# Kernel tuning notes

Measured on AMD Instinct MI355X. Metric: run time of the kernel, lower is better.

The kernel has to match this reference:

```python
import jax, jax.numpy as jnp
import numpy as np

N_NODES = 200000
N_EDGES = 3200000
NUM_GRAPHS = 100
NODES_PER_GRAPH = 2000
D_IN = 128
D_HID = 128
D_OUT = 64


def setup_inputs() -> dict:
    key = jax.random.key(0)
    ks = jax.random.split(key, 8)
    features = jax.random.normal(ks[0], (N_NODES, D_IN), dtype=jnp.float32)
    src = jax.random.randint(ks[1], (N_EDGES,), 0, N_NODES, dtype=jnp.int32)
    dst = jax.random.randint(ks[2], (N_EDGES,), 0, N_NODES, dtype=jnp.int32)
    to_fetch = jax.random.randint(ks[3], (NUM_GRAPHS,), 0, NODES_PER_GRAPH, dtype=jnp.int32)
    w1 = jax.random.normal(ks[4], (D_IN, D_HID), dtype=jnp.float32) * (1.0 / np.sqrt(D_IN))
    b1 = jnp.zeros((D_HID,), dtype=jnp.float32)
    w2 = jax.random.normal(ks[5], (D_HID, D_HID), dtype=jnp.float32) * (1.0 / np.sqrt(D_HID))
    b2 = jnp.zeros((D_HID,), dtype=jnp.float32)
    w3 = jax.random.normal(ks[6], (D_OUT, D_HID), dtype=jnp.float32) * (1.0 / np.sqrt(D_HID))  # F.linear weight [out, in]
    b3 = jnp.zeros((D_OUT,), dtype=jnp.float32)
    return {"features": features, "src": src, "dst": dst, "to_fetch": to_fetch,
            "w1": w1, "b1": b1, "w2": w2, "b2": b2, "w3": w3, "b3": b3}


def _graph_conv(h, src, dst, norm, w, b):
    # DGL GraphConv (in_feats == out_feats branch): normalize, aggregate copy_src/sum, matmul, normalize, bias, relu
    h = h * norm
    agg = jax.ops.segment_sum(h[src], dst, num_segments=N_NODES)  # [N, d]
    rst = jnp.matmul(agg, w) * norm + b
    return jax.nn.relu(rst)


def reference(features, src, dst, to_fetch, w1, b1, w2, b2, w3, b3):
    # in-degree based symmetric-ish norm (DGL uses in_degrees for both sides here)
    deg = jax.ops.segment_sum(jnp.ones((N_EDGES,), jnp.float32), dst, num_segments=N_NODES)
    norm = jnp.power(jnp.clip(deg, 1.0), -0.5)[:, None]  # [N, 1]
    h = _graph_conv(features, src, dst, norm, w1, b1)
    h = _graph_conv(h, src, dst, norm, w2, b2)
    # fetch one node per batched graph: offsets = cumsum of batch_num_nodes
    offsets = jnp.arange(NUM_GRAPHS, dtype=jnp.int32) * NODES_PER_GRAPH
    h = h[to_fetch + offsets]  # [B, d]
    h = jnp.matmul(h, w3.T) + b3  # F.linear
    return h
```

## Files before the change

kernel.cpp:

```cpp
#include <hip/hip_runtime.h>

#define NNODES 200000
#define NEDGES 3200000
#define NGRAPH 100
#define NPG    2000
#define D      128
#define DOUT   64
#define CAP1   4096
#define CAP2   8192
#define CAPE   65536
#define FBUF   2048

__global__ void init_kernel(int* deg, int* s1idx, unsigned char* need,
                            float* agg1, float* agg2, int* cnt) {
    int n = blockIdx.x * blockDim.x + threadIdx.x;
    if (n < NNODES) { deg[n] = 0; s1idx[n] = -1; need[n] = 0; }
    if (n < CAP1 * D) agg1[n] = 0.0f;
    if (n < NGRAPH * D) agg2[n] = 0.0f;
    if (n < 4) cnt[n] = 0;
}

__global__ void passA2(const int* __restrict__ src, const int4* __restrict__ dst4,
                       const int* __restrict__ to_fetch,
                       int* e2src, int* e2slot, int* s1idx, int* cnt) {
    __shared__ int tf[NGRAPH];
    __shared__ int lcnt, lbase;
    __shared__ int bufs[FBUF], bufj[FBUF];
    int tid = threadIdx.x;
    for (int i = tid; i < NGRAPH; i += blockDim.x) tf[i] = to_fetch[i];
    if (tid == 0) lcnt = 0;
    __syncthreads();
    const int NV = NEDGES / 4;
    int stride = gridDim.x * blockDim.x;
    int iters = (NV + stride - 1) / stride;
    int v0 = blockIdx.x * blockDim.x + tid;
    for (int it = 0; it < iters; ++it) {
        int v = v0 + it * stride;
        if (v < NV) {
            int4 d4 = dst4[v];
            int ds[4] = {d4.x, d4.y, d4.z, d4.w};
            #pragma unroll
            for (int q = 0; q < 4; ++q) {
                int d = ds[q];
                int slot = d / NPG;
                if (tf[slot] == d - slot * NPG) {
                    int s = src[v * 4 + q];
                    s1idx[s] = -2;
                    int p = atomicAdd(&lcnt, 1);
                    if (p < FBUF) { bufs[p] = s; bufj[p] = slot; }
                }
            }
        }
        __syncthreads();
        if (lcnt > FBUF - 1024) {
            int n = min(lcnt, FBUF);
            if (tid == 0) lbase = atomicAdd(&cnt[0], n);
            __syncthreads();
            for (int k = tid; k < n; k += blockDim.x) {
                int g = lbase + k;
                if (g < CAP2) { e2src[g] = bufs[k]; e2slot[g] = bufj[k]; }
            }
            __syncthreads();
            if (tid == 0) lcnt = 0;
            __syncthreads();
        }
    }
    int n = min(lcnt, FBUF);
    if (n > 0) {
        if (tid == 0) lbase = atomicAdd(&cnt[0], n);
        __syncthreads();
        for (int k = tid; k < n; k += blockDim.x) {
            int g = lbase + k;
            if (g < CAP2) { e2src[g] = bufs[k]; e2slot[g] = bufj[k]; }
        }
    }
}

__global__ void compact1(int* s1idx, int* s1nodes, unsigned char* need,
                         const int* __restrict__ to_fetch, int* cnt) {
    __shared__ int lcnt, lbase;
    __shared__ int buf[FBUF];
    int tid = threadIdx.x;
    if (blockIdx.x == 0 && tid < NGRAPH) need[to_fetch[tid] + tid * NPG] = 1;
    if (tid == 0) lcnt = 0;
    __syncthreads();
    int stride = gridDim.x * blockDim.x;
    int iters = (NNODES + stride - 1) / stride;
    int n0 = blockIdx.x * blockDim.x + tid;
    for (int it = 0; it < iters; ++it) {
        int n = n0 + it * stride;
        if (n < NNODES && s1idx[n] == -2) {
            int p = atomicAdd(&lcnt, 1);
            if (p < FBUF) buf[p] = n;
        }
        __syncthreads();
        if (lcnt > FBUF - 256) {
            int c = min(lcnt, FBUF);
            if (tid == 0) lbase = atomicAdd(&cnt[1], c);
            __syncthreads();
            for (int k = tid; k < c; k += blockDim.x) {
                int g = lbase + k; int node = buf[k];
                if (g < CAP1) { s1nodes[g] = node; s1idx[node] = g; need[node] = 1; }
                else s1idx[node] = -1;
            }
            __syncthreads();
            if (tid == 0) lcnt = 0;
            __syncthreads();
        }
    }
    int c = min(lcnt, FBUF);
    if (c > 0) {
        if (tid == 0) lbase = atomicAdd(&cnt[1], c);
        __syncthreads();
        for (int k = tid; k < c; k += blockDim.x) {
            int g = lbase + k; int node = buf[k];
            if (g < CAP1) { s1nodes[g] = node; s1idx[node] = g; need[node] = 1; }
            else s1idx[node] = -1;
        }
    }
}

__global__ void passB2(const int* __restrict__ src, const int4* __restrict__ dst4,
                       const int* __restrict__ s1idx, unsigned char* need,
                       int* e1src, int* e1j, int* cnt) {
    __shared__ int lcnt, lbase;
    __shared__ int bufs[FBUF], bufj[FBUF];
    int tid = threadIdx.x;
    if (tid == 0) lcnt = 0;
    __syncthreads();
    const int NV = NEDGES / 4;
    int stride = gridDim.x * blockDim.x;
    int iters = (NV + stride - 1) / stride;
    int v0 = blockIdx.x * blockDim.x + tid;
    for (int it = 0; it < iters; ++it) {
        int v = v0 + it * stride;
        if (v < NV) {
            int4 d4 = dst4[v];
            int ds[4] = {d4.x, d4.y, d4.z, d4.w};
            #pragma unroll
            for (int q = 0; q < 4; ++q) {
                int j = s1idx[ds[q]];
                if (j >= 0) {
                    int s = src[v * 4 + q];
                    need[s] = 1;
                    int p = atomicAdd(&lcnt, 1);
                    if (p < FBUF) { bufs[p] = s; bufj[p] = j; }
                }
            }
        }
        __syncthreads();
        if (lcnt > FBUF - 1024) {
            int n = min(lcnt, FBUF);
            if (tid == 0) lbase = atomicAdd(&cnt[2], n);
            __syncthreads();
            for (int k = tid; k < n; k += blockDim.x) {
                int g = lbase + k;
                if (g < CAPE) { e1src[g] = bufs[k]; e1j[g] = bufj[k]; }
            }
            __syncthreads();
            if (tid == 0) lcnt = 0;
            __syncthreads();
        }
    }
    int n = min(lcnt, FBUF);
    if (n > 0) {
        if (tid == 0) lbase = atomicAdd(&cnt[2], n);
        __syncthreads();
        for (int k = tid; k < n; k += blockDim.x) {
            int g = lbase + k;
            if (g < CAPE) { e1src[g] = bufs[k]; e1j[g] = bufj[k]; }
        }
    }
}

__global__ void passC(const int4* __restrict__ dst4, const unsigned char* __restrict__ need,
                      int* deg) {
    const int NV = NEDGES / 4;
    int stride = gridDim.x * blockDim.x;
    for (int v = blockIdx.x * blockDim.x + threadIdx.x; v < NV; v += stride) {
        int4 d4 = dst4[v];
        int ds[4] = {d4.x, d4.y, d4.z, d4.w};
        #pragma unroll
        for (int q = 0; q < 4; ++q)
            if (need[ds[q]]) atomicAdd(&deg[ds[q]], 1);
    }
}

__global__ void agg1_kernel(const int* __restrict__ e1src, const int* __restrict__ e1j,
                            const int* __restrict__ cnt, const int* __restrict__ deg,
                            const float* __restrict__ feat, float* agg1) {
    int t = threadIdx.x;
    int ne = min(cnt[2], CAPE);
    for (int e = blockIdx.x; e < ne; e += gridDim.x) {
        int s = e1src[e];
        float nm = rsqrtf(fmaxf((float)deg[s], 1.0f));
        float v = feat[(size_t)s * D + t] * nm;
        atomicAdd(&agg1[e1j[e] * D + t], v);
    }
}

__global__ void gemm1(const float* __restrict__ agg1, const float* __restrict__ w1,
                      const float* __restrict__ b1, const int* __restrict__ deg,
                      const int* __restrict__ s1nodes, const int* __restrict__ cnt,
                      float* h1n) {
    int nj = min(cnt[1], CAP1);
    int t = threadIdx.x;
    __shared__ float sa[D];
    for (int j = blockIdx.x; j < nj; j += gridDim.x) {
        __syncthreads();
        sa[t] = agg1[j * D + t];
        __syncthreads();
        float acc = 0.0f;
        #pragma unroll
        for (int k = 0; k < D; k++) acc += sa[k] * w1[k * D + t];
        float nm = rsqrtf(fmaxf((float)deg[s1nodes[j]], 1.0f));
        h1n[j * D + t] = fmaxf(acc * nm + b1[t], 0.0f) * nm;
    }
}

__global__ void agg2_kernel(const int* __restrict__ e2src, const int* __restrict__ e2slot,
                            const int* __restrict__ s1idx, const int* __restrict__ cnt,
                            const float* __restrict__ h1n, float* agg2) {
    int t = threadIdx.x;
    int ne = min(cnt[0], CAP2);
    for (int e = blockIdx.x; e < ne; e += gridDim.x) {
        int j = s1idx[e2src[e]];
        if (j >= 0) atomicAdd(&agg2[e2slot[e] * D + t], h1n[j * D + t]);
    }
}

__global__ void final_kernel(const float* __restrict__ agg2, const float* __restrict__ w2,
                             const float* __restrict__ b2, const int* __restrict__ deg,
                             const int* __restrict__ to_fetch,
                             const float* __restrict__ w3, const float* __restrict__ b3,
                             float* out) {
    int i = blockIdx.x;
    int t = threadIdx.x;
    __shared__ float sa[D], h2[D];
    sa[t] = agg2[i * D + t];
    __syncthreads();
    float acc = 0.0f;
    #pragma unroll
    for (int k = 0; k < D; k++) acc += sa[k] * w2[k * D + t];
    float nm = rsqrtf(fmaxf((float)deg[to_fetch[i] + i * NPG], 1.0f));
    h2[t] = fmaxf(acc * nm + b2[t], 0.0f);
    __syncthreads();
    if (t < DOUT) {
        float o = 0.0f;
        #pragma unroll
        for (int k = 0; k < D; k++) o += h2[k] * w3[t * D + k];
        out[i * DOUT + t] = o + b3[t];
    }
}

extern "C" void kernel_launch(void* const* d_in, const int* in_sizes, int n_in,
                              void* d_out, int out_size, void* d_ws, size_t ws_size,
                              hipStream_t stream) {
    const float* feat     = (const float*)d_in[0];
    const int*   src      = (const int*)  d_in[1];
    const int*   dst      = (const int*)  d_in[2];
    const int*   to_fetch = (const int*)  d_in[3];
    const float* w1       = (const float*)d_in[4];
    const float* b1       = (const float*)d_in[5];
    const float* w2       = (const float*)d_in[6];
    const float* b2       = (const float*)d_in[7];
    const float* w3       = (const float*)d_in[8];
    const float* b3       = (const float*)d_in[9];
    float* out = (float*)d_out;
    const int4* dst4 = (const int4*)dst;

    char* p = (char*)d_ws;
    int*   deg     = (int*)p;            p += (size_t)NNODES * 4;
    int*   s1idx   = (int*)p;            p += (size_t)NNODES * 4;
    int*   s1nodes = (int*)p;            p += (size_t)CAP1 * 4;
    int*   e2src   = (int*)p;            p += (size_t)CAP2 * 4;
    int*   e2slot  = (int*)p;            p += (size_t)CAP2 * 4;
    int*   e1src   = (int*)p;            p += (size_t)CAPE * 4;
    int*   e1j     = (int*)p;            p += (size_t)CAPE * 4;
    float* agg1    = (float*)p;          p += (size_t)CAP1 * D * 4;
    float* h1n     = (float*)p;          p += (size_t)CAP1 * D * 4;
    float* agg2    = (float*)p;          p += (size_t)NGRAPH * D * 4;
    int*   cnt     = (int*)p;            p += 16;
    unsigned char* need = (unsigned char*)p; p += (size_t)NNODES;

    int initN = CAP1 * D;
    init_kernel<<<(initN + 255) / 256, 256, 0, stream>>>(deg, s1idx, need, agg1, agg2, cnt);
    passA2<<<2048, 256, 0, stream>>>(src, dst4, to_fetch, e2src, e2slot, s1idx, cnt);
    compact1<<<512, 256, 0, stream>>>(s1idx, s1nodes, need, to_fetch, cnt);
    passB2<<<2048, 256, 0, stream>>>(src, dst4, s1idx, need, e1src, e1j, cnt);
    passC<<<2048, 256, 0, stream>>>(dst4, need, deg);
    agg1_kernel<<<2048, 128, 0, stream>>>(e1src, e1j, cnt, deg, feat, agg1);
    gemm1<<<CAP1, 128, 0, stream>>>(agg1, w1, b1, deg, s1nodes, cnt, h1n);
    agg2_kernel<<<1024, 128, 0, stream>>>(e2src, e2slot, s1idx, cnt, h1n, agg2);
    final_kernel<<<NGRAPH, 128, 0, stream>>>(agg2, w2, b2, deg, to_fetch, w3, b3, out);
}
```

Baseline: 128.0 us.

## Fuse pipeline stages into one persistent kernel with software grid barriers

Replaces eight separate kernel launches with one persistent kernel of 256 blocks that moves between stages through a hand-written grid barrier built on atomics. The aim is to remove per-launch overhead and the gaps between the short stages. It also replaces the compaction scan over all nodes with a wave-ballot compaction over only the collected edge sources. It batches several rows per block in the first GEMM and unrolls loads in the first aggregation. The risks are that the barrier deadlocks if the 256 blocks are not all resident at once, and that shrinking the shared buffer to 1024 entries with a single flush could drop entries if one block collects more than that.

```diff
diff --git a/kernel.cpp b/kernel.cpp
--- a/kernel.cpp
+++ b/kernel.cpp
@@ -9,247 +9,232 @@
 #define CAP1   4096
 #define CAP2   8192
 #define CAPE   65536
-#define FBUF   2048
-
-__global__ void init_kernel(int* deg, int* s1idx, unsigned char* need,
-                            float* agg1, float* agg2, int* cnt) {
+#define FBUF   1024
+#define NBLK   256
+#define NTHR   256
+
+__global__ void prek(int* deg, int* s1idx, unsigned char* need,
+                     float* agg1, float* agg2, int* cnt, int* bar) {
     int n = blockIdx.x * blockDim.x + threadIdx.x;
     if (n < NNODES) { deg[n] = 0; s1idx[n] = -1; need[n] = 0; }
     if (n < CAP1 * D) agg1[n] = 0.0f;
     if (n < NGRAPH * D) agg2[n] = 0.0f;
-    if (n < 4) cnt[n] = 0;
-}
-
-__global__ void passA2(const int* __restrict__ src, const int4* __restrict__ dst4,
-                       const int* __restrict__ to_fetch,
-                       int* e2src, int* e2slot, int* s1idx, int* cnt) {
+    if (n < 8) cnt[n] = 0;
+    if (n < 7 * 128) bar[n] = 0;
+}
+
+__device__ __forceinline__ void gridbar(int* bar, int bi) {
+    __syncthreads();
+    if (threadIdx.x == 0) {
+        __threadfence();
+        atomicAdd(&bar[bi * 128 + (blockIdx.x & 7) * 16], 1);
+        int s;
+        do {
+            s = 0;
+            #pragma unroll
+            for (int i = 0; i < 8; i++)
+                s += __hip_atomic_load(&bar[bi * 128 + i * 16],
+                                       __ATOMIC_RELAXED, __HIP_MEMORY_SCOPE_AGENT);
+        } while (s < NBLK);
+    }
+    __syncthreads();
+    __threadfence();
+}
+
+__global__ __launch_bounds__(NTHR) void mega(
+        const float* __restrict__ feat, const int* __restrict__ src,
+        const int4* __restrict__ dst4, const int* __restrict__ to_fetch,
+        const float* __restrict__ w1, const float* __restrict__ b1,
+        const float* __restrict__ w2, const float* __restrict__ b2,
+        const float* __restrict__ w3, const float* __restrict__ b3,
+        float* __restrict__ out,
+        int* deg, int* s1idx, unsigned char* need,
+        int* s1nodes, int* e2src, int* e2slot, int* e1src, int* e1j,
+        float* agg1, float* h1n, float* agg2, int* cnt, int* bar) {
+
+    const int tid = threadIdx.x;
+    const int bid = blockIdx.x;
+    const int gid = bid * NTHR + tid;
+    const int NV = NEDGES / 4;
+
     __shared__ int tf[NGRAPH];
     __shared__ int lcnt, lbase;
     __shared__ int bufs[FBUF], bufj[FBUF];
-    int tid = threadIdx.x;
-    for (int i = tid; i < NGRAPH; i += blockDim.x) tf[i] = to_fetch[i];
+    __shared__ float sa[8][D];
+
+    for (int i = tid; i < NGRAPH; i += NTHR) tf[i] = to_fetch[i];
     if (tid == 0) lcnt = 0;
     __syncthreads();
-    const int NV = NEDGES / 4;
-    int stride = gridDim.x * blockDim.x;
-    int iters = (NV + stride - 1) / stride;
-    int v0 = blockIdx.x * blockDim.x + tid;
-    for (int it = 0; it < iters; ++it) {
-        int v = v0 + it * stride;
-        if (v < NV) {
-            int4 d4 = dst4[v];
-            int ds[4] = {d4.x, d4.y, d4.z, d4.w};
-            #pragma unroll
-            for (int q = 0; q < 4; ++q) {
-                int d = ds[q];
-                int slot = d / NPG;
-                if (tf[slot] == d - slot * NPG) {
-                    int s = src[v * 4 + q];
-                    s1idx[s] = -2;
-                    int p = atomicAdd(&lcnt, 1);
-                    if (p < FBUF) { bufs[p] = s; bufj[p] = slot; }
-                }
-            }
-        }
-        __syncthreads();
-        if (lcnt > FBUF - 1024) {
-            int n = min(lcnt, FBUF);
-            if (tid == 0) lbase = atomicAdd(&cnt[0], n);
-            __syncthreads();
-            for (int k = tid; k < n; k += blockDim.x) {
-                int g = lbase + k;
-                if (g < CAP2) { e2src[g] = bufs[k]; e2slot[g] = bufj[k]; }
-            }
-            __syncthreads();
-            if (tid == 0) lcnt = 0;
-            __syncthreads();
-        }
-    }
-    int n = min(lcnt, FBUF);
-    if (n > 0) {
+    for (int v = gid; v < NV; v += NBLK * NTHR) {
+        int4 d4 = dst4[v];
+        int ds[4] = {d4.x, d4.y, d4.z, d4.w};
+        #pragma unroll
+        for (int q = 0; q < 4; ++q) {
+            int d = ds[q];
+            int slot = d / NPG;
+            if (tf[slot] == d - slot * NPG) {
+                int s = src[v * 4 + q];
+                s1idx[s] = -2;
+                int p = atomicAdd(&lcnt, 1);
+                if (p < FBUF) { bufs[p] = s; bufj[p] = slot; }
+            }
+        }
+    }
+    __syncthreads();
+    {
+        int n = min(lcnt, FBUF);
         if (tid == 0) lbase = atomicAdd(&cnt[0], n);
         __syncthreads();
-        for (int k = tid; k < n; k += blockDim.x) {
+        for (int k = tid; k < n; k += NTHR) {
             int g = lbase + k;
             if (g < CAP2) { e2src[g] = bufs[k]; e2slot[g] = bufj[k]; }
         }
-    }
-}
-
-__global__ void compact1(int* s1idx, int* s1nodes, unsigned char* need,
-                         const int* __restrict__ to_fetch, int* cnt) {
-    __shared__ int lcnt, lbase;
-    __shared__ int buf[FBUF];
-    int tid = threadIdx.x;
-    if (blockIdx.x == 0 && tid < NGRAPH) need[to_fetch[tid] + tid * NPG] = 1;
-    if (tid == 0) lcnt = 0;
-    __syncthreads();
-    int stride = gridDim.x * blockDim.x;
-    int iters = (NNODES + stride - 1) / stride;
-    int n0 = blockIdx.x * blockDim.x + tid;
-    for (int it = 0; it < iters; ++it) {
-        int n = n0 + it * stride;
-        if (n < NNODES && s1idx[n] == -2) {
-            int p = atomicAdd(&lcnt, 1);
-            if (p < FBUF) buf[p] = n;
-        }
-        __syncthreads();
-        if (lcnt > FBUF - 256) {
-            int c = min(lcnt, FBUF);
-            if (tid == 0) lbase = atomicAdd(&cnt[1], c);
-            __syncthreads();
-            for (int k = tid; k < c; k += blockDim.x) {
-                int g = lbase + k; int node = buf[k];
-                if (g < CAP1) { s1nodes[g] = node; s1idx[node] = g; need[node] = 1; }
-                else s1idx[node] = -1;
-            }
-            __syncthreads();
-            if (tid == 0) lcnt = 0;
-            __syncthreads();
-        }
-    }
-    int c = min(lcnt, FBUF);
-    if (c > 0) {
-        if (tid == 0) lbase = atomicAdd(&cnt[1], c);
-        __syncthreads();
-        for (int k = tid; k < c; k += blockDim.x) {
-            int g = lbase + k; int node = buf[k];
-            if (g < CAP1) { s1nodes[g] = node; s1idx[node] = g; need[node] = 1; }
-            else s1idx[node] = -1;
-        }
-    }
-}
-
-__global__ void passB2(const int* __restrict__ src, const int4* __restrict__ dst4,
-                       const int* __restrict__ s1idx, unsigned char* need,
-                       int* e1src, int* e1j, int* cnt) {
-    __shared__ int lcnt, lbase;
-    __shared__ int bufs[FBUF], bufj[FBUF];
-    int tid = threadIdx.x;
-    if (tid == 0) lcnt = 0;
-    __syncthreads();
-    const int NV = NEDGES / 4;
-    int stride = gridDim.x * blockDim.x;
-    int iters = (NV + stride - 1) / stride;
-    int v0 = blockIdx.x * blockDim.x + tid;
-    for (int it = 0; it < iters; ++it) {
-        int v = v0 + it * stride;
-        if (v < NV) {
-            int4 d4 = dst4[v];
-            int ds[4] = {d4.x, d4.y, d4.z, d4.w};
-            #pragma unroll
-            for (int q = 0; q < 4; ++q) {
-                int j = s1idx[ds[q]];
-                if (j >= 0) {
-                    int s = src[v * 4 + q];
-                    need[s] = 1;
-                    int p = atomicAdd(&lcnt, 1);
-                    if (p < FBUF) { bufs[p] = s; bufj[p] = j; }
+        __syncthreads();
+        if (tid == 0) lcnt = 0;
+    }
+    gridbar(bar, 0);
+
+    {
+        int n2 = min(cnt[0], CAP2);
+        if (bid == 0 && tid < NGRAPH) need[tf[tid] + tid * NPG] = 1;
+        for (int k = gid; k < n2; k += NBLK * NTHR) {
+            int s = e2src[k];
+            bool win = (atomicCAS(&s1idx[s], -2, -4) == -2);
+            unsigned long long mask = __ballot(win ? 1 : 0);
+            if (mask) {
+                int lane = tid & 63;
+                int lead = __ffsll(mask) - 1;
+                int nw = __popcll(mask);
+                int base = 0;
+                if (lane == lead) base = atomicAdd(&cnt[1], nw);
+                base = __shfl(base, lead, 64);
+                if (win) {
+                    int idx = base + __popcll(mask & ((1ull << lane) - 1ull));
+                    if (idx < CAP1) { s1idx[s] = idx; s1nodes[idx] = s; need[s] = 1; }
+                    else s1idx[s] = -1;
                 }
             }
         }
-        __syncthreads();
-        if (lcnt > FBUF - 1024) {
-            int n = min(lcnt, FBUF);
-            if (tid == 0) lbase = atomicAdd(&cnt[2], n);
-            __syncthreads();
-            for (int k = tid; k < n; k += blockDim.x) {
-                int g = lbase + k;
-                if (g < CAPE) { e1src[g] = bufs[k]; e1j[g] = bufj[k]; }
-            }
-            __syncthreads();
-            if (tid == 0) lcnt = 0;
-            __syncthreads();
-        }
-    }
-    int n = min(lcnt, FBUF);
-    if (n > 0) {
+    }
+    gridbar(bar, 1);
+
+    for (int v = gid; v < NV; v += NBLK * NTHR) {
+        int4 d4 = dst4[v];
+        int ds[4] = {d4.x, d4.y, d4.z, d4.w};
+        #pragma unroll
+        for (int q = 0; q < 4; ++q) {
+            int j = s1idx[ds[q]];
+            if (j >= 0) {
+                int s = src[v * 4 + q];
+                need[s] = 1;
+                int p = atomicAdd(&lcnt, 1);
+                if (p < FBUF) { bufs[p] = s; bufj[p] = j; }
+            }
+        }
+    }
+    __syncthreads();
+    {
+        int n = min(lcnt, FBUF);
         if (tid == 0) lbase = atomicAdd(&cnt[2], n);
         __syncthreads();
-        for (int k = tid; k < n; k += blockDim.x) {
+        for (int k = tid; k < n; k += NTHR) {
             int g = lbase + k;
             if (g < CAPE) { e1src[g] = bufs[k]; e1j[g] = bufj[k]; }
         }
     }
-}
-
-__global__ void passC(const int4* __restrict__ dst4, const unsigned char* __restrict__ need,
-                      int* deg) {
-    const int NV = NEDGES / 4;
-    int stride = gridDim.x * blockDim.x;
-    for (int v = blockIdx.x * blockDim.x + threadIdx.x; v < NV; v += stride) {
+    gridbar(bar, 2);
+
+    for (int v = gid; v < NV; v += NBLK * NTHR) {
         int4 d4 = dst4[v];
         int ds[4] = {d4.x, d4.y, d4.z, d4.w};
         #pragma unroll
         for (int q = 0; q < 4; ++q)
             if (need[ds[q]]) atomicAdd(&deg[ds[q]], 1);
     }
-}
-
-__global__ void agg1_kernel(const int* __restrict__ e1src, const int* __restrict__ e1j,
-                            const int* __restrict__ cnt, const int* __restrict__ deg,
-                            const float* __restrict__ feat, float* agg1) {
-    int t = threadIdx.x;
-    int ne = min(cnt[2], CAPE);
-    for (int e = blockIdx.x; e < ne; e += gridDim.x) {
-        int s = e1src[e];
-        float nm = rsqrtf(fmaxf((float)deg[s], 1.0f));
-        float v = feat[(size_t)s * D + t] * nm;
-        atomicAdd(&agg1[e1j[e] * D + t], v);
-    }
-}
-
-__global__ void gemm1(const float* __restrict__ agg1, const float* __restrict__ w1,
-                      const float* __restrict__ b1, const int* __restrict__ deg,
-                      const int* __restrict__ s1nodes, const int* __restrict__ cnt,
-                      float* h1n) {
-    int nj = min(cnt[1], CAP1);
-    int t = threadIdx.x;
-    __shared__ float sa[D];
-    for (int j = blockIdx.x; j < nj; j += gridDim.x) {
-        __syncthreads();
-        sa[t] = agg1[j * D + t];
-        __syncthreads();
-        float acc = 0.0f;
-        #pragma unroll
-        for (int k = 0; k < D; k++) acc += sa[k] * w1[k * D + t];
-        float nm = rsqrtf(fmaxf((float)deg[s1nodes[j]], 1.0f));
-        h1n[j * D + t] = fmaxf(acc * nm + b1[t], 0.0f) * nm;
-    }
-}
-
-__global__ void agg2_kernel(const int* __restrict__ e2src, const int* __restrict__ e2slot,
-                            const int* __restrict__ s1idx, const int* __restrict__ cnt,
-                            const float* __restrict__ h1n, float* agg2) {
-    int t = threadIdx.x;
-    int ne = min(cnt[0], CAP2);
-    for (int e = blockIdx.x; e < ne; e += gridDim.x) {
-        int j = s1idx[e2src[e]];
-        if (j >= 0) atomicAdd(&agg2[e2slot[e] * D + t], h1n[j * D + t]);
-    }
-}
-
-__global__ void final_kernel(const float* __restrict__ agg2, const float* __restrict__ w2,
-                             const float* __restrict__ b2, const int* __restrict__ deg,
-                             const int* __restrict__ to_fetch,
-                             const float* __restrict__ w3, const float* __restrict__ b3,
-                             float* out) {
-    int i = blockIdx.x;
-    int t = threadIdx.x;
-    __shared__ float sa[D], h2[D];
-    sa[t] = agg2[i * D + t];
-    __syncthreads();
-    float acc = 0.0f;
-    #pragma unroll
-    for (int k = 0; k < D; k++) acc += sa[k] * w2[k * D + t];
-    float nm = rsqrtf(fmaxf((float)deg[to_fetch[i] + i * NPG], 1.0f));
-    h2[t] = fmaxf(acc * nm + b2[t], 0.0f);
-    __syncthreads();
-    if (t < DOUT) {
-        float o = 0.0f;
-        #pragma unroll
-        for (int k = 0; k < D; k++) o += h2[k] * w3[t * D + k];
-        out[i * DOUT + t] = o + b3[t];
+    gridbar(bar, 3);
+
+    {
+        int ne = min(cnt[2], CAPE);
+        int col = tid & 127, sub = tid >> 7;
+        for (int base = bid * 2 + sub; base < ne; base += NBLK * 2 * 8) {
+            float v[8]; int jj[8];
+            #pragma unroll
+            for (int u = 0; u < 8; ++u) {
+                int e = base + u * NBLK * 2; jj[u] = -1;
+                if (e < ne) {
+                    int s = e1src[e];
+                    jj[u] = e1j[e];
+                    v[u] = feat[(size_t)s * D + col] * rsqrtf(fmaxf((float)deg[s], 1.0f));
+                }
+            }
+            #pragma unroll
+            for (int u = 0; u < 8; ++u)
+                if (jj[u] >= 0) atomicAdd(&agg1[jj[u] * D + col], v[u]);
+        }
+    }
+    gridbar(bar, 4);
+
+    {
+        int nj = min(cnt[1], CAP1);
+        int col = tid & 127, half = tid >> 7;
+        for (int g = bid; g * 8 < nj; g += NBLK) {
+            __syncthreads();
+            for (int x = tid; x < 8 * D; x += NTHR) {
+                int r = x >> 7, c = x & 127, row = g * 8 + r;
+                sa[r][c] = (row < nj) ? agg1[row * D + c] : 0.0f;
+            }
+            __syncthreads();
+            int r0 = half * 4;
+            float a0 = 0, a1 = 0, a2 = 0, a3 = 0;
+            #pragma unroll 4
+            for (int k = 0; k < D; k++) {
+                float w = w1[k * D + col];
+                a0 += sa[r0 + 0][k] * w; a1 += sa[r0 + 1][k] * w;
+                a2 += sa[r0 + 2][k] * w; a3 += sa[r0 + 3][k] * w;
+            }
+            float bb = b1[col];
+            float accs[4] = {a0, a1, a2, a3};
+            #pragma unroll
+            for (int i = 0; i < 4; i++) {
+                int row = g * 8 + r0 + i;
+                if (row < nj) {
+                    float nm = rsqrtf(fmaxf((float)deg[s1nodes[row]], 1.0f));
+                    h1n[row * D + col] = fmaxf(accs[i] * nm + bb, 0.0f) * nm;
+                }
+            }
+        }
+    }
+    gridbar(bar, 5);
+
+    {
+        int n2 = min(cnt[0], CAP2);
+        int col = tid & 127, sub = tid >> 7;
+        for (int e = bid * 2 + sub; e < n2; e += NBLK * 2) {
+            int j = s1idx[e2src[e]];
+            if (j >= 0) atomicAdd(&agg2[e2slot[e] * D + col], h1n[j * D + col]);
+        }
+    }
+    gridbar(bar, 6);
+
+    if (bid < NGRAPH) {
+        int i = bid;
+        __shared__ float sv[D], h2[D];
+        if (tid < D) sv[tid] = agg2[i * D + tid];
+        __syncthreads();
+        if (tid < D) {
+            float acc = 0.0f;
+            #pragma unroll 4
+            for (int k = 0; k < D; k++) acc += sv[k] * w2[k * D + tid];
+            float nm = rsqrtf(fmaxf((float)deg[tf[i] + i * NPG], 1.0f));
+            h2[tid] = fmaxf(acc * nm + b2[tid], 0.0f);
+        }
+        __syncthreads();
+        if (tid < DOUT) {
+            float o = 0.0f;
+            #pragma unroll 4
+            for (int k = 0; k < D; k++) o += h2[k] * w3[tid * D + k];
+            out[i * DOUT + tid] = o + b3[tid];
+        }
     }
 }
 
@@ -280,17 +265,12 @@
     float* agg1    = (float*)p;          p += (size_t)CAP1 * D * 4;
     float* h1n     = (float*)p;          p += (size_t)CAP1 * D * 4;
     float* agg2    = (float*)p;          p += (size_t)NGRAPH * D * 4;
-    int*   cnt     = (int*)p;            p += 16;
+    int*   cnt     = (int*)p;            p += 64;
+    int*   bar     = (int*)p;            p += 7 * 128 * 4;
     unsigned char* need = (unsigned char*)p; p += (size_t)NNODES;
 
-    int initN = CAP1 * D;
-    init_kernel<<<(initN + 255) / 256, 256, 0, stream>>>(deg, s1idx, need, agg1, agg2, cnt);
-    passA2<<<2048, 256, 0, stream>>>(src, dst4, to_fetch, e2src, e2slot, s1idx, cnt);
-    compact1<<<512, 256, 0, stream>>>(s1idx, s1nodes, need, to_fetch, cnt);
-    passB2<<<2048, 256, 0, stream>>>(src, dst4, s1idx, need, e1src, e1j, cnt);
-    passC<<<2048, 256, 0, stream>>>(dst4, need, deg);
-    agg1_kernel<<<2048, 128, 0, stream>>>(e1src, e1j, cnt, deg, feat, agg1);
-    gemm1<<<CAP1, 128, 0, stream>>>(agg1, w1, b1, deg, s1nodes, cnt, h1n);
-    agg2_kernel<<<1024, 128, 0, stream>>>(e2src, e2slot, s1idx, cnt, h1n, agg2);
-    final_kernel<<<NGRAPH, 128, 0, stream>>>(agg2, w2, b2, deg, to_fetch, w3, b3, out);
-}
+    prek<<<(CAP1 * D + 255) / 256, 256, 0, stream>>>(deg, s1idx, need, agg1, agg2, cnt, bar);
+    mega<<<NBLK, NTHR, 0, stream>>>(feat, src, dst4, to_fetch, w1, b1, w2, b2, w3, b3,
+                                    out, deg, s1idx, need, s1nodes, e2src, e2slot,
+                                    e1src, e1j, agg1, h1n, agg2, cnt, bar);
+}
```

New measurement: 307.9 us. +140.6%, slower.

## Fuse frontier compaction into edge pass and merge layer-2 aggregation with final

Applied to the files above, without the earlier changes.

Removes the separate compaction kernel. Nodes of the first-layer frontier are now claimed inline with atomicCAS plus a wave-level ballot and prefix allocation during the destination scan. The layer-2 scatter-add kernel is merged into the final kernel, with each graph block gathering its own edges instead of using global atomics, so the agg2 buffer and its zeroing go away. gemm1 now processes 8 rows per block so each weight load is reused across 4 rows. The per-iteration block sync and flush in the edge pass are dropped and FBUF is halved, so a block that collects more than 1024 edges would silently drop them, and each final block now scans all layer-2 edges.

```diff
diff --git a/kernel.cpp b/kernel.cpp
--- a/kernel.cpp
+++ b/kernel.cpp
@@ -9,64 +9,61 @@
 #define CAP1   4096
 #define CAP2   8192
 #define CAPE   65536
-#define FBUF   2048
-
-__global__ void init_kernel(int* deg, int* s1idx, unsigned char* need,
-                            float* agg1, float* agg2, int* cnt) {
+#define FBUF   1024
+
+__global__ void prek(int* deg, int* s1idx, unsigned char* need, float* agg1, int* cnt) {
     int n = blockIdx.x * blockDim.x + threadIdx.x;
     if (n < NNODES) { deg[n] = 0; s1idx[n] = -1; need[n] = 0; }
     if (n < CAP1 * D) agg1[n] = 0.0f;
-    if (n < NGRAPH * D) agg2[n] = 0.0f;
-    if (n < 4) cnt[n] = 0;
-}
-
-__global__ void passA2(const int* __restrict__ src, const int4* __restrict__ dst4,
+    if (n < 8) cnt[n] = 0;
+}
+
+__global__ void passAC(const int* __restrict__ src, const int4* __restrict__ dst4,
                        const int* __restrict__ to_fetch,
-                       int* e2src, int* e2slot, int* s1idx, int* cnt) {
+                       int* e2src, int* e2slot, int* s1idx, int* s1nodes,
+                       unsigned char* need, int* cnt) {
     __shared__ int tf[NGRAPH];
     __shared__ int lcnt, lbase;
     __shared__ int bufs[FBUF], bufj[FBUF];
     int tid = threadIdx.x;
     for (int i = tid; i < NGRAPH; i += blockDim.x) tf[i] = to_fetch[i];
+    if (blockIdx.x == 0 && tid < NGRAPH) need[to_fetch[tid] + tid * NPG] = 1;
     if (tid == 0) lcnt = 0;
     __syncthreads();
     const int NV = NEDGES / 4;
     int stride = gridDim.x * blockDim.x;
-    int iters = (NV + stride - 1) / stride;
-    int v0 = blockIdx.x * blockDim.x + tid;
-    for (int it = 0; it < iters; ++it) {
-        int v = v0 + it * stride;
-        if (v < NV) {
-            int4 d4 = dst4[v];
-            int ds[4] = {d4.x, d4.y, d4.z, d4.w};
-            #pragma unroll
-            for (int q = 0; q < 4; ++q) {
-                int d = ds[q];
-                int slot = d / NPG;
-                if (tf[slot] == d - slot * NPG) {
-                    int s = src[v * 4 + q];
-                    s1idx[s] = -2;
-                    int p = atomicAdd(&lcnt, 1);
-                    if (p < FBUF) { bufs[p] = s; bufj[p] = slot; }
+    for (int v = blockIdx.x * blockDim.x + tid; v < NV; v += stride) {
+        int4 d4 = dst4[v];
+        int ds[4] = {d4.x, d4.y, d4.z, d4.w};
+        #pragma unroll
+        for (int q = 0; q < 4; ++q) {
+            int d = ds[q];
+            int slot = d / NPG;
+            if (tf[slot] == d - slot * NPG) {
+                int s = src[v * 4 + q];
+                int p = atomicAdd(&lcnt, 1);
+                if (p < FBUF) { bufs[p] = s; bufj[p] = slot; }
+                bool win = (atomicCAS(&s1idx[s], -1, -2) == -1);
+                unsigned long long mask = __ballot(win ? 1 : 0);
+                if (mask) {
+                    int lane = tid & 63;
+                    int lead = __ffsll(mask) - 1;
+                    int nw = __popcll(mask);
+                    int base = 0;
+                    if (lane == lead) base = atomicAdd(&cnt[1], nw);
+                    base = __shfl(base, lead, 64);
+                    if (win) {
+                        int idx = base + __popcll(mask & ((1ull << lane) - 1ull));
+                        if (idx < CAP1) { s1idx[s] = idx; s1nodes[idx] = s; need[s] = 1; }
+                        else s1idx[s] = -1;
+                    }
                 }
             }
         }
-        __syncthreads();
-        if (lcnt > FBUF - 1024) {
-            int n = min(lcnt, FBUF);
-            if (tid == 0) lbase = atomicAdd(&cnt[0], n);
-            __syncthreads();
-            for (int k = tid; k < n; k += blockDim.x) {
-                int g = lbase + k;
-                if (g < CAP2) { e2src[g] = bufs[k]; e2slot[g] = bufj[k]; }
-            }
-            __syncthreads();
-            if (tid == 0) lcnt = 0;
-            __syncthreads();
-        }
-    }
-    int n = min(lcnt, FBUF);
-    if (n > 0) {
+    }
+    __syncthreads();
+    {
+        int n = min(lcnt, FBUF);
         if (tid == 0) lbase = atomicAdd(&cnt[0], n);
         __syncthreads();
         for (int k = tid; k < n; k += blockDim.x) {
@@ -76,53 +73,9 @@
     }
 }
 
-__global__ void compact1(int* s1idx, int* s1nodes, unsigned char* need,
-                         const int* __restrict__ to_fetch, int* cnt) {
-    __shared__ int lcnt, lbase;
-    __shared__ int buf[FBUF];
-    int tid = threadIdx.x;
-    if (blockIdx.x == 0 && tid < NGRAPH) need[to_fetch[tid] + tid * NPG] = 1;
-    if (tid == 0) lcnt = 0;
-    __syncthreads();
-    int stride = gridDim.x * blockDim.x;
-    int iters = (NNODES + stride - 1) / stride;
-    int n0 = blockIdx.x * blockDim.x + tid;
-    for (int it = 0; it < iters; ++it) {
-        int n = n0 + it * stride;
-        if (n < NNODES && s1idx[n] == -2) {
-            int p = atomicAdd(&lcnt, 1);
-            if (p < FBUF) buf[p] = n;
-        }
-        __syncthreads();
-        if (lcnt > FBUF - 256) {
-            int c = min(lcnt, FBUF);
-            if (tid == 0) lbase = atomicAdd(&cnt[1], c);
-            __syncthreads();
-            for (int k = tid; k < c; k += blockDim.x) {
-                int g = lbase + k; int node = buf[k];
-                if (g < CAP1) { s1nodes[g] = node; s1idx[node] = g; need[node] = 1; }
-                else s1idx[node] = -1;
-            }
-            __syncthreads();
-            if (tid == 0) lcnt = 0;
-            __syncthreads();
-        }
-    }
-    int c = min(lcnt, FBUF);
-    if (c > 0) {
-        if (tid == 0) lbase = atomicAdd(&cnt[1], c);
-        __syncthreads();
-        for (int k = tid; k < c; k += blockDim.x) {
-            int g = lbase + k; int node = buf[k];
-            if (g < CAP1) { s1nodes[g] = node; s1idx[node] = g; need[node] = 1; }
-            else s1idx[node] = -1;
-        }
-    }
-}
-
-__global__ void passB2(const int* __restrict__ src, const int4* __restrict__ dst4,
-                       const int* __restrict__ s1idx, unsigned char* need,
-                       int* e1src, int* e1j, int* cnt) {
+__global__ void passB(const int* __restrict__ src, const int4* __restrict__ dst4,
+                      const int* __restrict__ s1idx, unsigned char* need,
+                      int* e1src, int* e1j, int* cnt) {
     __shared__ int lcnt, lbase;
     __shared__ int bufs[FBUF], bufj[FBUF];
     int tid = threadIdx.x;
@@ -204,50 +157,73 @@
                       const int* __restrict__ s1nodes, const int* __restrict__ cnt,
                       float* h1n) {
     int nj = min(cnt[1], CAP1);
-    int t = threadIdx.x;
-    __shared__ float sa[D];
-    for (int j = blockIdx.x; j < nj; j += gridDim.x) {
-        __syncthreads();
-        sa[t] = agg1[j * D + t];
-        __syncthreads();
-        float acc = 0.0f;
+    int tid = threadIdx.x;
+    int col = tid & 127, half = tid >> 7;
+    __shared__ float sa[8][D];
+    for (int g = blockIdx.x; g * 8 < nj; g += gridDim.x) {
+        __syncthreads();
+        for (int x = tid; x < 8 * D; x += blockDim.x) {
+            int r = x >> 7, c = x & 127, row = g * 8 + r;
+            sa[r][c] = (row < nj) ? agg1[row * D + c] : 0.0f;
+        }
+        __syncthreads();
+        int r0 = half * 4;
+        float a0 = 0, a1 = 0, a2 = 0, a3 = 0;
+        #pragma unroll 4
+        for (int k = 0; k < D; k++) {
+            float w = w1[k * D + col];
+            a0 += sa[r0 + 0][k] * w; a1 += sa[r0 + 1][k] * w;
+            a2 += sa[r0 + 2][k] * w; a3 += sa[r0 + 3][k] * w;
+        }
+        float bb = b1[col];
+        float accs[4] = {a0, a1, a2, a3};
         #pragma unroll
-        for (int k = 0; k < D; k++) acc += sa[k] * w1[k * D + t];
-        float nm = rsqrtf(fmaxf((float)deg[s1nodes[j]], 1.0f));
-        h1n[j * D + t] = fmaxf(acc * nm + b1[t], 0.0f) * nm;
-    }
-}
-
-__global__ void agg2_kernel(const int* __restrict__ e2src, const int* __restrict__ e2slot,
-                            const int* __restrict__ s1idx, const int* __restrict__ cnt,
-                            const float* __restrict__ h1n, float* agg2) {
-    int t = threadIdx.x;
-    int ne = min(cnt[0], CAP2);
-    for (int e = blockIdx.x; e < ne; e += gridDim.x) {
-        int j = s1idx[e2src[e]];
-        if (j >= 0) atomicAdd(&agg2[e2slot[e] * D + t], h1n[j * D + t]);
-    }
-}
-
-__global__ void final_kernel(const float* __restrict__ agg2, const float* __restrict__ w2,
-                             const float* __restrict__ b2, const int* __restrict__ deg,
-                             const int* __restrict__ to_fetch,
-                             const float* __restrict__ w3, const float* __restrict__ b3,
-                             float* out) {
+        for (int i = 0; i < 4; i++) {
+            int row = g * 8 + r0 + i;
+            if (row < nj) {
+                float nm = rsqrtf(fmaxf((float)deg[s1nodes[row]], 1.0f));
+                h1n[row * D + col] = fmaxf(accs[i] * nm + bb, 0.0f) * nm;
+            }
+        }
+    }
+}
+
+__global__ void agg2final(const int* __restrict__ e2src, const int* __restrict__ e2slot,
+                          const int* __restrict__ s1idx, const int* __restrict__ cnt,
+                          const float* __restrict__ h1n, const int* __restrict__ deg,
+                          const int* __restrict__ to_fetch,
+                          const float* __restrict__ w2, const float* __restrict__ b2,
+                          const float* __restrict__ w3, const float* __restrict__ b3,
+                          float* __restrict__ out) {
     int i = blockIdx.x;
     int t = threadIdx.x;
-    __shared__ float sa[D], h2[D];
-    sa[t] = agg2[i * D + t];
-    __syncthreads();
+    __shared__ float sv[D], h2[D];
+    __shared__ int lj[256];
+    __shared__ int lc;
+    if (t == 0) lc = 0;
+    __syncthreads();
+    int ne2 = min(cnt[0], CAP2);
+    for (int e = t; e < ne2; e += blockDim.x) {
+        if (e2slot[e] == i) {
+            int j = s1idx[e2src[e]];
+            if (j >= 0) { int p = atomicAdd(&lc, 1); if (p < 256) lj[p] = j; }
+        }
+    }
+    __syncthreads();
+    int m = min(lc, 256);
     float acc = 0.0f;
-    #pragma unroll
-    for (int k = 0; k < D; k++) acc += sa[k] * w2[k * D + t];
+    for (int k = 0; k < m; ++k) acc += h1n[lj[k] * D + t];
+    sv[t] = acc;
+    __syncthreads();
+    float a2 = 0.0f;
+    #pragma unroll 4
+    for (int k = 0; k < D; k++) a2 += sv[k] * w2[k * D + t];
     float nm = rsqrtf(fmaxf((float)deg[to_fetch[i] + i * NPG], 1.0f));
-    h2[t] = fmaxf(acc * nm + b2[t], 0.0f);
+    h2[t] = fmaxf(a2 * nm + b2[t], 0.0f);
     __syncthreads();
     if (t < DOUT) {
         float o = 0.0f;
-        #pragma unroll
+        #pragma unroll 4
         for (int k = 0; k < D; k++) o += h2[k] * w3[t * D + k];
         out[i * DOUT + t] = o + b3[t];
     }
@@ -279,18 +255,16 @@
     int*   e1j     = (int*)p;            p += (size_t)CAPE * 4;
     float* agg1    = (float*)p;          p += (size_t)CAP1 * D * 4;
     float* h1n     = (float*)p;          p += (size_t)CAP1 * D * 4;
-    float* agg2    = (float*)p;          p += (size_t)NGRAPH * D * 4;
-    int*   cnt     = (int*)p;            p += 16;
+    int*   cnt     = (int*)p;            p += 64;
     unsigned char* need = (unsigned char*)p; p += (size_t)NNODES;
 
-    int initN = CAP1 * D;
-    init_kernel<<<(initN + 255) / 256, 256, 0, stream>>>(deg, s1idx, need, agg1, agg2, cnt);
-    passA2<<<2048, 256, 0, stream>>>(src, dst4, to_fetch, e2src, e2slot, s1idx, cnt);
-    compact1<<<512, 256, 0, stream>>>(s1idx, s1nodes, need, to_fetch, cnt);
-    passB2<<<2048, 256, 0, stream>>>(src, dst4, s1idx, need, e1src, e1j, cnt);
+    prek<<<(CAP1 * D + 255) / 256, 256, 0, stream>>>(deg, s1idx, need, agg1, cnt);
+    passAC<<<2048, 256, 0, stream>>>(src, dst4, to_fetch, e2src, e2slot,
+                                     s1idx, s1nodes, need, cnt);
+    passB<<<2048, 256, 0, stream>>>(src, dst4, s1idx, need, e1src, e1j, cnt);
     passC<<<2048, 256, 0, stream>>>(dst4, need, deg);
     agg1_kernel<<<2048, 128, 0, stream>>>(e1src, e1j, cnt, deg, feat, agg1);
-    gemm1<<<CAP1, 128, 0, stream>>>(agg1, w1, b1, deg, s1nodes, cnt, h1n);
-    agg2_kernel<<<1024, 128, 0, stream>>>(e2src, e2slot, s1idx, cnt, h1n, agg2);
-    final_kernel<<<NGRAPH, 128, 0, stream>>>(agg2, w2, b2, deg, to_fetch, w3, b3, out);
-}
+    gemm1<<<512, 256, 0, stream>>>(agg1, w1, b1, deg, s1nodes, cnt, h1n);
+    agg2final<<<NGRAPH, 128, 0, stream>>>(e2src, e2slot, s1idx, cnt, h1n, deg,
+                                          to_fetch, w2, b2, w3, b3, out);
+}
```

Result: slower. 168.0 us (+31.3%).
